# Performance work log

Hardware: AMD Instinct MI355X
Metric: run time of the kernel (lower is better)

The kernel has to match this reference:

```python
import jax, jax.numpy as jnp
import numpy as np

N_NODES = 50000
N_EDGES = 800000
IN_DIM = 128
HID_DIM = 128
OUT_DIM = 128


def setup_inputs() -> dict:
    key = jax.random.key(0)
    k = jax.random.split(key, 8)
    x = jax.random.normal(k[0], (N_NODES, IN_DIM), dtype=jnp.float32)
    edge_index = jax.random.randint(k[1], (2, N_EDGES), 0, N_NODES, dtype=jnp.int64)
    edge_weight = jax.random.uniform(k[2], (N_EDGES,), dtype=jnp.float32)
    # GCNConv params: weight [in, out] (glorot-ish), bias [out]
    W1 = jax.random.normal(k[3], (IN_DIM, HID_DIM), dtype=jnp.float32) / np.sqrt(IN_DIM)
    b1 = jnp.zeros((HID_DIM,), dtype=jnp.float32)
    W2 = jax.random.normal(k[4], (HID_DIM, OUT_DIM), dtype=jnp.float32) / np.sqrt(HID_DIM)
    b2 = jnp.zeros((OUT_DIM,), dtype=jnp.float32)
    return {"x": x, "edge_index": edge_index, "edge_weight": edge_weight,
            "W1": W1, "b1": b1, "W2": W2, "b2": b2}


def gcn_conv(x, W, b, src, dst, ew, n_nodes):
    """PyG GCNConv: add self-loops (weight 1), symmetric D^-1/2 (A+I) D^-1/2 norm."""
    h = x @ W  # [N, out]
    deg = jax.ops.segment_sum(ew, dst, num_segments=n_nodes) + 1.0  # +1 for self loop
    dis = jnp.where(deg > 0, jax.lax.rsqrt(deg), 0.0)  # deg^{-1/2}
    norm = dis[src] * ew * dis[dst]  # [E]
    msg = h[src] * norm[:, None]  # gather + weight -> [E, out]
    agg = jax.ops.segment_sum(msg, dst, num_segments=n_nodes)
    # self-loop contribution: norm_ii = dis[i] * 1 * dis[i]
    agg = agg + h * (dis * dis)[:, None]
    return agg + b


def reference(x, edge_index, edge_weight, W1, b1, W2, b2):
    src, dst = edge_index[0], edge_index[1]
    n = x.shape[0]
    h = gcn_conv(x, W1, b1, src, dst, edge_weight, n)
    h = jax.nn.relu(h)
    out = gcn_conv(h, W2, b2, src, dst, edge_weight, n)
    return out
```

## Files before the change

### kernel.cpp

```cpp
#include <hip/hip_runtime.h>

#define NDIM 128

typedef __attribute__((ext_vector_type(8))) short bf16x8;
typedef __attribute__((ext_vector_type(4))) float floatx4;

__device__ __forceinline__ float bflo(unsigned v){ return __uint_as_float(v << 16); }
__device__ __forceinline__ float bfhi(unsigned v){ return __uint_as_float(v & 0xffff0000u); }
__device__ __forceinline__ unsigned f2bf(float f){
  unsigned u = __float_as_uint(f);
  return (u + 0x7fffu + ((u >> 16) & 1u)) >> 16;
}

__global__ void k_init(unsigned long long* pk, int n){
  int i = blockIdx.x * blockDim.x + threadIdx.x;
  if (i < n) pk[i] = 0ULL;
}

__global__ void k_deg(const int* __restrict__ ei, const float* __restrict__ ew,
                      unsigned long long* pk, int E){
  int e = blockIdx.x * blockDim.x + threadIdx.x;
  if (e >= E) return;
  int d = ei[E + e];
  unsigned fx = (unsigned)__float2uint_rn(ew[e] * 1048576.0f);
  atomicAdd(&pk[d], (1ULL << 44) | (unsigned long long)fx);
}

__global__ __launch_bounds__(1024) void k_scan1(const unsigned long long* __restrict__ pk,
                                                int* __restrict__ off,
                                                int* __restrict__ bsum, int n){
  __shared__ int wsum[16];
  int t = threadIdx.x;
  int i = blockIdx.x * 1024 + t;
  int c = (i < n) ? (int)(pk[i] >> 44) : 0;
  int lane = t & 63, w = t >> 6;
  int v = c;
  #pragma unroll
  for (int d = 1; d < 64; d <<= 1){ int u = __shfl_up(v, d); if (lane >= d) v += u; }
  if (lane == 63) wsum[w] = v;
  __syncthreads();
  if (w == 0){
    int sv = (lane < 16) ? wsum[lane] : 0;
    #pragma unroll
    for (int d = 1; d < 16; d <<= 1){ int u = __shfl_up(sv, d); if (lane >= d) sv += u; }
    if (lane < 16) wsum[lane] = sv;
  }
  __syncthreads();
  int base = (w > 0) ? wsum[w - 1] : 0;
  if (i < n) off[i] = base + v - c;
  if (t == 1023) bsum[blockIdx.x] = wsum[15];
}

__global__ void k_scan2(int* bsum, int nb){
  int lane = threadIdx.x & 63;
  int c = (lane < nb) ? bsum[lane] : 0;
  int v = c;
  #pragma unroll
  for (int d = 1; d < 64; d <<= 1){ int u = __shfl_up(v, d); if (lane >= d) v += u; }
  if (lane < nb) bsum[lane] = v - c;
}

__global__ __launch_bounds__(1024) void k_scan3(int* __restrict__ off, int* __restrict__ cur,
                                                const int* __restrict__ bsum,
                                                const unsigned long long* __restrict__ pk,
                                                float* __restrict__ dis, int n, int E){
  int i = blockIdx.x * 1024 + threadIdx.x;
  if (i == 0) off[n] = E;
  if (i >= n) return;
  int o = off[i] + bsum[blockIdx.x];
  off[i] = o; cur[i] = o;
  float deg = 1.0f + (float)(pk[i] & ((1ULL << 44) - 1)) * (1.0f / 1048576.0f);
  dis[i] = rsqrtf(deg);
}

__global__ void k_place(const int* __restrict__ ei, const float* __restrict__ ew,
                        const float* __restrict__ dis, int* cur, unsigned* edges, int E){
  int e = blockIdx.x * blockDim.x + threadIdx.x;
  if (e >= E) return;
  int s = ei[e], d = ei[E + e];
  int p = atomicAdd(&cur[d], 1);
  edges[p] = (f2bf(dis[s] * ew[e] * dis[d]) << 16) | (unsigned)s;
}

__global__ void k_wprep(const float* __restrict__ W, unsigned short* __restrict__ Wp){
  int t = blockIdx.x * 256 + threadIdx.x;
  int k = t >> 7, n = t & 127;
  int kt = k >> 5, kq = (k >> 3) & 3, j = k & 7;
  int Lb = kq * 16 + (n & 15);
  Wp[(((kt * 8 + (n >> 4)) * 64) + Lb) * 8 + j] = (unsigned short)f2bf(W[t]);
}

template<int XF32>
__global__ __launch_bounds__(256) void k_gemm_mfma(const void* __restrict__ Xv,
                                                   const unsigned short* __restrict__ Wp,
                                                   unsigned short* __restrict__ Hout,
                                                   int ntiles){
  __shared__ unsigned short Wb[4 * 8 * 64 * 8];
  int tid = threadIdx.x;
  for (int t = tid; t < 2048; t += 256)
    ((uint4*)Wb)[t] = ((const uint4*)Wp)[t];
  __syncthreads();

  int w = tid >> 6, L = tid & 63;
  int m = L & 15, q = L >> 4;
  for (int tile = blockIdx.x * 4 + w; tile < ntiles; tile += gridDim.x * 4){
    size_t row = (size_t)tile * 16 + m;
    floatx4 acc[8] = {};
    #pragma unroll
    for (int kt = 0; kt < 4; ++kt){
      bf16x8 a;
      if (XF32){
        const float* xp = (const float*)Xv + row * NDIM + kt * 32 + q * 8;
        float4 a0 = *(const float4*)xp;
        float4 a1 = *(const float4*)(xp + 4);
        unsigned short* as = (unsigned short*)&a;
        as[0] = f2bf(a0.x); as[1] = f2bf(a0.y); as[2] = f2bf(a0.z); as[3] = f2bf(a0.w);
        as[4] = f2bf(a1.x); as[5] = f2bf(a1.y); as[6] = f2bf(a1.z); as[7] = f2bf(a1.w);
      } else {
        a = *(const bf16x8*)((const unsigned short*)Xv + row * NDIM + kt * 32 + q * 8);
      }
      #pragma unroll
      for (int ct = 0; ct < 8; ++ct){
        bf16x8 b = *(const bf16x8*)&Wb[((kt * 8 + ct) * 64 + L) * 8];
        acc[ct] = __builtin_amdgcn_mfma_f32_16x16x32_bf16(a, b, acc[ct], 0, 0, 0);
      }
    }
    #pragma unroll
    for (int ct = 0; ct < 8; ++ct){
      #pragma unroll
      for (int r = 0; r < 4; ++r){
        size_t orow = (size_t)tile * 16 + q * 4 + r;
        Hout[orow * NDIM + ct * 16 + m] = (unsigned short)f2bf(acc[ct][r]);
      }
    }
  }
}

template<int OUT_F32>
__global__ __launch_bounds__(256) void k_agg(const unsigned short* __restrict__ H,
                                             const int* __restrict__ off,
                                             const unsigned* __restrict__ edges,
                                             const float* __restrict__ dis,
                                             const float* __restrict__ bias,
                                             void* __restrict__ out,
                                             int n, int do_relu){
  int g = threadIdx.x >> 6, L = threadIdx.x & 63;
  int i = blockIdx.x * 4 + g;
  if (i >= n) return;
  float di = dis[i];
  float2 bv = ((const float2*)bias)[L];
  unsigned hv = ((const unsigned*)(H + (size_t)i * NDIM))[L];
  float acc0 = bv.x + bflo(hv) * di * di;
  float acc1 = bv.y + bfhi(hv) * di * di;
  int p = off[i], p1 = off[i + 1];
  while (p + 8 <= p1){
    unsigned e[8], h[8];
    #pragma unroll
    for (int j = 0; j < 8; ++j) e[j] = edges[p + j];
    #pragma unroll
    for (int j = 0; j < 8; ++j)
      h[j] = ((const unsigned*)(H + (size_t)(e[j] & 0xFFFF) * NDIM))[L];
    #pragma unroll
    for (int j = 0; j < 8; ++j){
      float w = bfhi(e[j]);
      acc0 = fmaf(bflo(h[j]), w, acc0);
      acc1 = fmaf(bfhi(h[j]), w, acc1);
    }
    p += 8;
  }
  for (; p < p1; ++p){
    unsigned e = edges[p];
    unsigned h2 = ((const unsigned*)(H + (size_t)(e & 0xFFFF) * NDIM))[L];
    float w = bfhi(e);
    acc0 = fmaf(bflo(h2), w, acc0);
    acc1 = fmaf(bfhi(h2), w, acc1);
  }
  if (do_relu){ acc0 = fmaxf(acc0, 0.f); acc1 = fmaxf(acc1, 0.f); }
  if (OUT_F32){
    ((float2*)((float*)out + (size_t)i * NDIM))[L] = make_float2(acc0, acc1);
  } else {
    ((unsigned*)((unsigned short*)out + (size_t)i * NDIM))[L] = (f2bf(acc1) << 16) | f2bf(acc0);
  }
}

extern "C" void kernel_launch(void* const* d_in, const int* in_sizes, int n_in,
                              void* d_out, int out_size, void* d_ws, size_t ws_size,
                              hipStream_t stream){
  const float* x  = (const float*)d_in[0];
  const int*   ei = (const int*)  d_in[1];
  const float* ew = (const float*)d_in[2];
  const float* W1 = (const float*)d_in[3];
  const float* b1 = (const float*)d_in[4];
  const float* W2 = (const float*)d_in[5];
  const float* b2 = (const float*)d_in[6];
  float* out = (float*)d_out;
  int N = in_sizes[0] / NDIM;
  int E = in_sizes[2];
  int nb = (N + 1023) / 1024;
  int ntiles = N / 16;

  char* p = (char*)d_ws;
  auto alloc = [&](size_t b) -> char* { char* r = p; p += (b + 255) & ~(size_t)255; return r; };
  unsigned long long* pk = (unsigned long long*)alloc((size_t)N * 8);
  float*    dis   = (float*)   alloc((size_t)N * 4);
  int*      cur   = (int*)     alloc((size_t)N * 4);
  int*      off   = (int*)     alloc((size_t)(N + 1) * 4);
  int*      bsum  = (int*)     alloc((size_t)64 * 4);
  unsigned short* Wp1 = (unsigned short*)alloc(NDIM * NDIM * 2);
  unsigned short* Wp2 = (unsigned short*)alloc(NDIM * NDIM * 2);
  unsigned* edges = (unsigned*)alloc((size_t)E * 4);
  unsigned short* R = (unsigned short*)alloc((size_t)N * NDIM * 2);
  unsigned short* H1 = (unsigned short*)d_out;

  k_init <<<(N + 255) / 256, 256, 0, stream>>>(pk, N);
  k_deg  <<<(E + 255) / 256, 256, 0, stream>>>(ei, ew, pk, E);
  k_scan1<<<nb, 1024, 0, stream>>>(pk, off, bsum, N);
  k_scan2<<<1, 64, 0, stream>>>(bsum, nb);
  k_scan3<<<nb, 1024, 0, stream>>>(off, cur, bsum, pk, dis, N, E);
  k_place<<<(E + 255) / 256, 256, 0, stream>>>(ei, ew, dis, cur, edges, E);
  k_wprep<<<64, 256, 0, stream>>>(W1, Wp1);
  k_wprep<<<64, 256, 0, stream>>>(W2, Wp2);

  k_gemm_mfma<1><<<512, 256, 0, stream>>>(x, Wp1, H1, ntiles);
  k_agg<0> <<<(N + 3) / 4, 256, 0, stream>>>(H1, off, edges, dis, b1, R, N, 1);
  k_gemm_mfma<0><<<512, 256, 0, stream>>>(R, Wp2, R, ntiles);
  k_agg<1> <<<(N + 3) / 4, 256, 0, stream>>>(R, off, edges, dis, b2, out, N, 0);
}
```

Baseline: 265.9 us.

## Merge small prep kernels, fold scan2 into scan3, retune agg and gemm launches

Merges the pk zeroing and both weight-packing kernels into one launch, and folds the block-sum scan into the final scan kernel so each block recomputes its base in one wavefront. This cuts the number of kernel launches and the gaps between them. It also doubles the aggregation block to 512 threads (8 nodes per block) and sizes the GEMM grid to one tile per wave instead of a fixed 512 blocks. The GEMM change removes the grid-stride reuse of the staged weight tile, so every block loads W into LDS itself.

New measurement: 269.8 us. About the same (+1.5%).

```diff
diff --git a/kernel.cpp b/kernel.cpp
--- a/kernel.cpp
+++ b/kernel.cpp
@@ -12,9 +12,20 @@
   return (u + 0x7fffu + ((u >> 16) & 1u)) >> 16;
 }
 
-__global__ void k_init(unsigned long long* pk, int n){
-  int i = blockIdx.x * blockDim.x + threadIdx.x;
+__global__ void k_prep0(unsigned long long* __restrict__ pk,
+                        const float* __restrict__ W1, const float* __restrict__ W2,
+                        unsigned short* __restrict__ Wp1, unsigned short* __restrict__ Wp2,
+                        int n){
+  int i = blockIdx.x * 256 + threadIdx.x;
   if (i < n) pk[i] = 0ULL;
+  if (i < NDIM * NDIM){
+    int k = i >> 7, c = i & 127;
+    int kt = k >> 5, kq = (k >> 3) & 3, j = k & 7;
+    int Lb = kq * 16 + (c & 15);
+    int idx = (((kt * 8 + (c >> 4)) * 64) + Lb) * 8 + j;
+    Wp1[idx] = (unsigned short)f2bf(W1[i]);
+    Wp2[idx] = (unsigned short)f2bf(W2[i]);
+  }
 }
 
 __global__ void k_deg(const int* __restrict__ ei, const float* __restrict__ ew,
@@ -51,23 +62,24 @@
   if (t == 1023) bsum[blockIdx.x] = wsum[15];
 }
 
-__global__ void k_scan2(int* bsum, int nb){
-  int lane = threadIdx.x & 63;
-  int c = (lane < nb) ? bsum[lane] : 0;
-  int v = c;
-  #pragma unroll
-  for (int d = 1; d < 64; d <<= 1){ int u = __shfl_up(v, d); if (lane >= d) v += u; }
-  if (lane < nb) bsum[lane] = v - c;
-}
-
-__global__ __launch_bounds__(1024) void k_scan3(int* __restrict__ off, int* __restrict__ cur,
-                                                const int* __restrict__ bsum,
-                                                const unsigned long long* __restrict__ pk,
-                                                float* __restrict__ dis, int n, int E){
-  int i = blockIdx.x * 1024 + threadIdx.x;
+__global__ __launch_bounds__(1024) void k_scan23(int* __restrict__ off, int* __restrict__ cur,
+                                                 const int* __restrict__ bsum,
+                                                 const unsigned long long* __restrict__ pk,
+                                                 float* __restrict__ dis, int n, int E, int nb){
+  __shared__ int sBase;
+  int t = threadIdx.x;
+  if (t < 64){
+    int c2 = (t < nb) ? bsum[t] : 0;
+    int v2 = c2;
+    #pragma unroll
+    for (int d = 1; d < 64; d <<= 1){ int u = __shfl_up(v2, d); if (t >= d) v2 += u; }
+    if (t == (int)blockIdx.x) sBase = v2 - c2;
+  }
+  __syncthreads();
+  int i = blockIdx.x * 1024 + t;
   if (i == 0) off[n] = E;
   if (i >= n) return;
-  int o = off[i] + bsum[blockIdx.x];
+  int o = off[i] + sBase;
   off[i] = o; cur[i] = o;
   float deg = 1.0f + (float)(pk[i] & ((1ULL << 44) - 1)) * (1.0f / 1048576.0f);
   dis[i] = rsqrtf(deg);
@@ -80,14 +92,6 @@
   int s = ei[e], d = ei[E + e];
   int p = atomicAdd(&cur[d], 1);
   edges[p] = (f2bf(dis[s] * ew[e] * dis[d]) << 16) | (unsigned)s;
-}
-
-__global__ void k_wprep(const float* __restrict__ W, unsigned short* __restrict__ Wp){
-  int t = blockIdx.x * 256 + threadIdx.x;
-  int k = t >> 7, n = t & 127;
-  int kt = k >> 5, kq = (k >> 3) & 3, j = k & 7;
-  int Lb = kq * 16 + (n & 15);
-  Wp[(((kt * 8 + (n >> 4)) * 64) + Lb) * 8 + j] = (unsigned short)f2bf(W[t]);
 }
 
 template<int XF32>
@@ -137,7 +141,7 @@
 }
 
 template<int OUT_F32>
-__global__ __launch_bounds__(256) void k_agg(const unsigned short* __restrict__ H,
+__global__ __launch_bounds__(512) void k_agg(const unsigned short* __restrict__ H,
                                              const int* __restrict__ off,
                                              const unsigned* __restrict__ edges,
                                              const float* __restrict__ dis,
@@ -145,7 +149,7 @@
                                              void* __restrict__ out,
                                              int n, int do_relu){
   int g = threadIdx.x >> 6, L = threadIdx.x & 63;
-  int i = blockIdx.x * 4 + g;
+  int i = blockIdx.x * 8 + g;
   if (i >= n) return;
   float di = dis[i];
   float2 bv = ((const float2*)bias)[L];
@@ -212,17 +216,15 @@
   unsigned short* R = (unsigned short*)alloc((size_t)N * NDIM * 2);
   unsigned short* H1 = (unsigned short*)d_out;
 
-  k_init <<<(N + 255) / 256, 256, 0, stream>>>(pk, N);
+  k_prep0<<<(N + 255) / 256, 256, 0, stream>>>(pk, W1, W2, Wp1, Wp2, N);
   k_deg  <<<(E + 255) / 256, 256, 0, stream>>>(ei, ew, pk, E);
   k_scan1<<<nb, 1024, 0, stream>>>(pk, off, bsum, N);
-  k_scan2<<<1, 64, 0, stream>>>(bsum, nb);
-  k_scan3<<<nb, 1024, 0, stream>>>(off, cur, bsum, pk, dis, N, E);
+  k_scan23<<<nb, 1024, 0, stream>>>(off, cur, bsum, pk, dis, N, E, nb);
   k_place<<<(E + 255) / 256, 256, 0, stream>>>(ei, ew, dis, cur, edges, E);
-  k_wprep<<<64, 256, 0, stream>>>(W1, Wp1);
-  k_wprep<<<64, 256, 0, stream>>>(W2, Wp2);
-
-  k_gemm_mfma<1><<<512, 256, 0, stream>>>(x, Wp1, H1, ntiles);
-  k_agg<0> <<<(N + 3) / 4, 256, 0, stream>>>(H1, off, edges, dis, b1, R, N, 1);
-  k_gemm_mfma<0><<<512, 256, 0, stream>>>(R, Wp2, R, ntiles);
-  k_agg<1> <<<(N + 3) / 4, 256, 0, stream>>>(R, off, edges, dis, b2, out, N, 0);
-}
+
+  int gg = (ntiles + 3) / 4;
+  k_gemm_mfma<1><<<gg, 256, 0, stream>>>(x, Wp1, H1, ntiles);
+  k_agg<0> <<<(N + 7) / 8, 512, 0, stream>>>(H1, off, edges, dis, b1, R, N, 1);
+  k_gemm_mfma<0><<<gg, 256, 0, stream>>>(R, Wp2, R, ntiles);
+  k_agg<1> <<<(N + 7) / 8, 512, 0, stream>>>(R, off, edges, dis, b2, out, N, 0);
+}
```
